# Performance work log

Measured on AMD Instinct MI355X. Metric: run time of the kernel, lower is better.

## Reference

```python
import jax, jax.numpy as jnp
import numpy as np

N_ENT, N_REL = 100000, 500
D1, D2 = 200, 200
OC, FW = 32, 9            # out_channels, filt_w (filt_h = 1, in_channels = 1)
B = 4096
W_IN = 2 * D1             # 400 = concat(e1, e2)
W_OUT = W_IN - FW + 1     # 392
FC_LEN = OC * W_OUT       # 12544
FC1_LEN = OC * FW         # 288
EPS = 1e-5


def setup_inputs() -> dict:
    key = jax.random.key(0)
    ks = jax.random.split(key, 8)
    return {
        "e1_idx": jax.random.randint(ks[0], (B,), 0, N_ENT),
        "r_idx": jax.random.randint(ks[1], (B,), 0, N_REL),
        "e2_idx": jax.random.randint(ks[2], (B,), 0, N_ENT),
        "E_table": jax.random.normal(ks[3], (N_ENT, D1), jnp.float32) * 0.1,
        "R_table": jax.random.normal(ks[4], (N_REL, D2), jnp.float32) * 0.1,
        "bn0_gamma": jnp.ones((1,), jnp.float32),
        "bn0_beta": jnp.zeros((1,), jnp.float32),
        "bn0_mean": jnp.zeros((1,), jnp.float32),
        "bn0_var": jnp.ones((1,), jnp.float32),
        "fc1_w": jax.random.normal(ks[5], (FC1_LEN, D2), jnp.float32) * 0.05,
        "fc1_b": jnp.zeros((FC1_LEN,), jnp.float32),
        "bn1_gamma": jnp.ones((OC,), jnp.float32),
        "bn1_beta": jnp.zeros((OC,), jnp.float32),
        "bn1_mean": jnp.zeros((OC,), jnp.float32),
        "bn1_var": jnp.ones((OC,), jnp.float32),
        "fc_w": jax.random.normal(ks[6], (W_IN, FC_LEN), jnp.float32) * 0.02,
        "fc_b": jnp.zeros((W_IN,), jnp.float32),
        "bn2_gamma": jnp.ones((W_IN,), jnp.float32),
        "bn2_beta": jnp.zeros((W_IN,), jnp.float32),
        "bn2_mean": jnp.zeros((W_IN,), jnp.float32),
        "bn2_var": jnp.ones((W_IN,), jnp.float32),
        "fc2_w": jax.random.normal(ks[7], (1, W_IN), jnp.float32) * 0.05,
        "fc2_b": jnp.zeros((1,), jnp.float32),
        "bias": jnp.zeros((1,), jnp.float32),
    }


def reference(e1_idx, r_idx, e2_idx, E_table, R_table,
              bn0_gamma, bn0_beta, bn0_mean, bn0_var,
              fc1_w, fc1_b,
              bn1_gamma, bn1_beta, bn1_mean, bn1_var,
              fc_w, fc_b,
              bn2_gamma, bn2_beta, bn2_mean, bn2_var,
              fc2_w, fc2_b, bias):
    # Embedding lookups; E = concat(e1, e2) along feature dim -> [B, 400]
    e1 = E_table[e1_idx]
    e2 = E_table[e2_idx]
    E = jnp.concatenate([e1, e2], axis=-1)

    # bn0 over the single input channel (eval-mode batchnorm)
    x = (E - bn0_mean[0]) * (bn0_gamma[0] / jnp.sqrt(bn0_var[0] + EPS)) + bn0_beta[0]

    # Hypernetwork: per-example conv filters [B, OC, FW]
    r = R_table[r_idx]
    k = (r @ fc1_w.T + fc1_b).reshape(-1, OC, FW)

    # Grouped (per-example) 1x9 convolution, valid padding.
    # Sliding windows: [B, W_OUT, FW] (loop over FW=9 taps only)
    xw = jnp.stack([x[:, j:j + W_OUT] for j in range(FW)], axis=-1)
    conv = jnp.einsum('bwj,boj->bow', xw, k)  # [B, OC, W_OUT]

    # bn1 over OC channels (eval mode)
    inv1 = bn1_gamma / jnp.sqrt(bn1_var + EPS)
    y = (conv - bn1_mean[None, :, None]) * inv1[None, :, None] + bn1_beta[None, :, None]

    # flatten in [B, OC, 1, W_OUT] contiguous order -> [B, OC*W_OUT]
    flat = y.reshape(y.shape[0], -1)

    h = flat @ fc_w.T + fc_b                                   # [B, 400]
    h = (h - bn2_mean) * (bn2_gamma / jnp.sqrt(bn2_var + EPS)) + bn2_beta
    out = jnp.tanh(h @ fc2_w.T + fc2_b) + bias                 # [B, 1]
    return out
```

## Files before the change

kernel.cpp:

```cpp
#include <hip/hip_runtime.h>

#define BATCH   4096
#define N_REL   500
#define D1      200
#define W_IN    400
#define OC      32
#define FW      9
#define W_OUT   392
#define FC_LEN  12544
#define FC1_LEN 288
#define EPS     1e-5f

#define OSPLIT  8
#define OCH     50
#define WBLK    49


__global__ __launch_bounds__(320)
void krel(const float* __restrict__ R, const float* __restrict__ fc1w,
          const float* __restrict__ fc1b,
          const float* __restrict__ g1, const float* __restrict__ v1,
          float* __restrict__ KR)
{
    __shared__ float rs[D1];
    const int rel = blockIdx.x;
    const int t = threadIdx.x;
    if (t < D1) rs[t] = R[(size_t)rel * D1 + t];
    __syncthreads();
    if (t < FC1_LEN) {
        const float4* wrow = (const float4*)(fc1w + (size_t)t * D1);
        float acc = fc1b[t];
        #pragma unroll 10
        for (int c = 0; c < D1 / 4; ++c) {
            float4 wv = wrow[c];
            acc += rs[c * 4 + 0] * wv.x + rs[c * 4 + 1] * wv.y
                 + rs[c * 4 + 2] * wv.z + rs[c * 4 + 3] * wv.w;
        }
        const int oc = t / FW;
        KR[(size_t)rel * FC1_LEN + t] = acc * (g1[oc] * rsqrtf(v1[oc] + EPS));
    }
}

__global__ __launch_bounds__(256)
void wpart_k(const float* __restrict__ fcw, const float* __restrict__ g2,
             const float* __restrict__ v2, const float* __restrict__ fc2w,
             float* __restrict__ wpart)
{
    __shared__ float wts[OCH];
    const int t = threadIdx.x;
    const int k = blockIdx.x * 256 + t;
    const int o0 = blockIdx.y * OCH;
    if (t < OCH) {
        const int o = o0 + t;
        wts[t] = fc2w[o] * g2[o] * rsqrtf(v2[o] + EPS);
    }
    __syncthreads();
    float acc = 0.f;
    #pragma unroll 10
    for (int i = 0; i < OCH; ++i)
        acc += fcw[(size_t)(o0 + i) * FC_LEN + k] * wts[i];
    wpart[blockIdx.y * FC_LEN + k] = acc;
}

__global__ __launch_bounds__(256)
void wsum_k(const float* __restrict__ wpart,
            const float* __restrict__ g1, const float* __restrict__ b1,
            const float* __restrict__ m1, const float* __restrict__ v1,
            const float* __restrict__ g2, const float* __restrict__ b2,
            const float* __restrict__ m2, const float* __restrict__ v2,
            const float* __restrict__ fcb, const float* __restrict__ fc2w,
            const float* __restrict__ fc2b,
            float* __restrict__ wbig, float* __restrict__ c3part)
{
    __shared__ float red[256];
    const int t = threadIdx.x;
    const int k = blockIdx.x * 256 + t;
    float w8 = 0.f;
    #pragma unroll
    for (int y = 0; y < OSPLIT; ++y) w8 += wpart[y * FC_LEN + k];
    wbig[k] = w8;
    const int oc = k / W_OUT;
    const float inv1 = g1[oc] * rsqrtf(v1[oc] + EPS);
    float pc = (b1[oc] - m1[oc] * inv1) * w8;
    if (blockIdx.x == 0) {
        for (int o = t; o < W_IN; o += 256) {
            const float s2 = g2[o] * rsqrtf(v2[o] + EPS);
            pc += (b2[o] - m2[o] * s2 + fcb[o] * s2) * fc2w[o];
        }
        if (t == 0) pc += fc2b[0];
    }
    red[t] = pc;
    __syncthreads();
    #pragma unroll
    for (int s = 128; s > 0; s >>= 1) {
        if (t < s) red[t] += red[t + s];
        __syncthreads();
    }
    if (t == 0) c3part[blockIdx.x] = red[0];
}

__global__ __launch_bounds__(256)
void prel_k(const float* __restrict__ KR, const float* __restrict__ wbig,
            const float* __restrict__ c3part,
            const float* __restrict__ g0, const float* __restrict__ b0,
            const float* __restrict__ m0p, const float* __restrict__ v0,
            float* __restrict__ Ps, float* __restrict__ crel)
{
    __shared__ __align__(16) float wls[FC_LEN];
    __shared__ float kfs[FC1_LEN];
    __shared__ float red[256];
    const int rel = blockIdx.x;
    const int t = threadIdx.x;

    for (int i = t; i < FC_LEN / 4; i += 256)
        *(float4*)(wls + i * 4) = *(const float4*)(wbig + i * 4);
    for (int i = t; i < FC1_LEN; i += 256)
        kfs[i] = KR[(size_t)rel * FC1_LEN + i];
    __syncthreads();

    const float s0 = g0[0] * rsqrtf(v0[0] + EPS);
    const float t0 = b0[0] - m0p[0] * s0;

    float lsum = 0.f;
    for (int d = t; d < W_IN; d += 256) {
        const int jlo = (d > W_OUT - 1) ? d - (W_OUT - 1) : 0;
        const int jhi = (d < FW - 1) ? d : (FW - 1);
        float p = 0.f;
        for (int oc = 0; oc < OC; ++oc) {
            const float* wb = wls + oc * W_OUT + d;
            const float* kk = kfs + oc * FW;
            for (int j = jlo; j <= jhi; ++j)
                p += kk[j] * wb[-j];
        }
        lsum += p;
        Ps[(size_t)rel * W_IN + d] = s0 * p;
    }
    red[t] = lsum;
    __syncthreads();
    #pragma unroll
    for (int s = 128; s > 0; s >>= 1) {
        if (t < s) red[t] += red[t + s];
        __syncthreads();
    }
    if (t == 0) {
        float cg = 0.f;
        for (int i = 0; i < WBLK; ++i) cg += c3part[i];
        crel[rel] = t0 * red[0] + cg;
    }
}

__global__ __launch_bounds__(256)
void final_k(const int* __restrict__ e1i, const int* __restrict__ ri,
             const int* __restrict__ e2i,
             const float* __restrict__ E, const float* __restrict__ Ps,
             const float* __restrict__ crel, const float* __restrict__ bias,
             float* __restrict__ out)
{
    const int wave = threadIdx.x >> 6, lane = threadIdx.x & 63;
    const int e = blockIdx.x * 4 + wave;
    const int i1 = e1i[e], i2 = e2i[e], rel = ri[e];
    const float* P  = Ps + (size_t)rel * W_IN;
    const float* E1 = E + (size_t)i1 * D1;
    const float* E2 = E + (size_t)i2 * D1;
    float acc = 0.f;
    for (int d = lane; d < D1; d += 64) acc += E1[d] * P[d];
    for (int d = lane; d < D1; d += 64) acc += E2[d] * P[D1 + d];
    #pragma unroll
    for (int off = 32; off > 0; off >>= 1) acc += __shfl_down(acc, off);
    if (lane == 0) out[e] = tanhf(acc + crel[rel]) + bias[0];
}

extern "C" void kernel_launch(void* const* d_in, const int* in_sizes, int n_in,
                              void* d_out, int out_size, void* d_ws, size_t ws_size,
                              hipStream_t stream)
{
    const int*   e1i  = (const int*)d_in[0];
    const int*   ri   = (const int*)d_in[1];
    const int*   e2i  = (const int*)d_in[2];
    const float* E    = (const float*)d_in[3];
    const float* R    = (const float*)d_in[4];
    const float* g0   = (const float*)d_in[5];
    const float* b0   = (const float*)d_in[6];
    const float* m0p  = (const float*)d_in[7];
    const float* v0   = (const float*)d_in[8];
    const float* fc1w = (const float*)d_in[9];
    const float* fc1b = (const float*)d_in[10];
    const float* g1   = (const float*)d_in[11];
    const float* b1   = (const float*)d_in[12];
    const float* m1   = (const float*)d_in[13];
    const float* v1   = (const float*)d_in[14];
    const float* fcw  = (const float*)d_in[15];
    const float* fcb  = (const float*)d_in[16];
    const float* g2   = (const float*)d_in[17];
    const float* b2   = (const float*)d_in[18];
    const float* m2   = (const float*)d_in[19];
    const float* v2   = (const float*)d_in[20];
    const float* fc2w = (const float*)d_in[21];
    const float* fc2b = (const float*)d_in[22];
    const float* bias = (const float*)d_in[23];

    char* ws = (char*)d_ws;
    float* KR     = (float*)(ws + 0);
    float* wpart  = (float*)(ws + 576000);
    float* wbig   = (float*)(ws + 977408);
    float* c3part = (float*)(ws + 1027584);
    float* Ps     = (float*)(ws + 1027840);
    float* crel   = (float*)(ws + 1827840);
    (void)ws_size; (void)in_sizes; (void)n_in; (void)out_size;

    krel<<<N_REL, 320, 0, stream>>>(R, fc1w, fc1b, g1, v1, KR);
    wpart_k<<<dim3(WBLK, OSPLIT), 256, 0, stream>>>(fcw, g2, v2, fc2w, wpart);
    wsum_k<<<WBLK, 256, 0, stream>>>(wpart, g1, b1, m1, v1, g2, b2, m2, v2,
                                     fcb, fc2w, fc2b, wbig, c3part);
    prel_k<<<N_REL, 256, 0, stream>>>(KR, wbig, c3part, g0, b0, m0p, v0, Ps, crel);
    final_k<<<BATCH / 4, 256, 0, stream>>>(e1i, ri, e2i, E, Ps, crel, bias,
                                           (float*)d_out);
}
```

Measured before the change: 211.2 us.

## Fuse five-stage pipeline into one cooperative persistent kernel with grid syncs

Replaces the five separate kernel launches with one cooperative kernel of 512 blocks that runs each stage in turn, separated by grid-wide syncs. The first stage interleaves the krel and wpart work units. The aim is to remove launch overhead and inter-kernel gaps. In exchange, every block carries about 52KB of shared memory, grid.sync has its own cost, and the later stages leave many blocks idle. The original multi-launch path is kept as a fallback if the cooperative launch fails.

```diff
diff --git a/kernel.cpp b/kernel.cpp
--- a/kernel.cpp
+++ b/kernel.cpp
@@ -1,4 +1,7 @@
 #include <hip/hip_runtime.h>
+#include <hip/hip_cooperative_groups.h>
+
+namespace cg = cooperative_groups;
 
 #define BATCH   4096
 #define N_REL   500
@@ -14,6 +17,152 @@
 #define OSPLIT  8
 #define OCH     50
 #define WBLK    49
+#define GRID    512
+
+
+struct Params {
+    const int *e1i, *ri, *e2i;
+    const float *E, *R;
+    const float *g0, *b0, *m0p, *v0;
+    const float *fc1w, *fc1b;
+    const float *g1, *b1, *m1, *v1;
+    const float *fcw, *fcb;
+    const float *g2, *b2, *m2, *v2;
+    const float *fc2w, *fc2b, *bias;
+    float *KR, *wpart, *wbig, *c3part, *Ps, *crel, *out;
+};
+
+__global__ __launch_bounds__(256)
+void fused_k(Params p)
+{
+    cg::grid_group grid = cg::this_grid();
+    __shared__ __align__(16) float smem[13088];
+    const int t  = threadIdx.x;
+    const int bx = blockIdx.x;
+
+    for (int u = bx; u < N_REL + OSPLIT * WBLK; u += GRID) {
+        if (u < N_REL) {
+            float* rs = smem;
+            if (t < D1) rs[t] = p.R[(size_t)u * D1 + t];
+            __syncthreads();
+            for (int i = t; i < FC1_LEN; i += 256) {
+                const float4* wrow = (const float4*)(p.fc1w + (size_t)i * D1);
+                float acc = p.fc1b[i];
+                #pragma unroll 10
+                for (int c = 0; c < D1 / 4; ++c) {
+                    float4 wv = wrow[c];
+                    acc += rs[c * 4 + 0] * wv.x + rs[c * 4 + 1] * wv.y
+                         + rs[c * 4 + 2] * wv.z + rs[c * 4 + 3] * wv.w;
+                }
+                const int oc = i / FW;
+                p.KR[(size_t)u * FC1_LEN + i] = acc * (p.g1[oc] * rsqrtf(p.v1[oc] + EPS));
+            }
+            __syncthreads();
+        } else {
+            const int v = u - N_REL;
+            const int y = v / WBLK, kb = v - y * WBLK;
+            const int o0 = y * OCH;
+            float* wts = smem;
+            if (t < OCH) {
+                const int o = o0 + t;
+                wts[t] = p.fc2w[o] * p.g2[o] * rsqrtf(p.v2[o] + EPS);
+            }
+            __syncthreads();
+            const int k = kb * 256 + t;
+            float acc = 0.f;
+            #pragma unroll 10
+            for (int i = 0; i < OCH; ++i)
+                acc += p.fcw[(size_t)(o0 + i) * FC_LEN + k] * wts[i];
+            p.wpart[y * FC_LEN + k] = acc;
+            __syncthreads();
+        }
+    }
+    grid.sync();
+
+    if (bx < WBLK) {
+        float* red = smem;
+        const int k = bx * 256 + t;
+        float w8 = 0.f;
+        #pragma unroll
+        for (int y = 0; y < OSPLIT; ++y) w8 += p.wpart[y * FC_LEN + k];
+        p.wbig[k] = w8;
+        const int oc = k / W_OUT;
+        const float inv1 = p.g1[oc] * rsqrtf(p.v1[oc] + EPS);
+        float pc = (p.b1[oc] - p.m1[oc] * inv1) * w8;
+        if (bx == 0) {
+            for (int o = t; o < W_IN; o += 256) {
+                const float s2 = p.g2[o] * rsqrtf(p.v2[o] + EPS);
+                pc += (p.b2[o] - p.m2[o] * s2 + p.fcb[o] * s2) * p.fc2w[o];
+            }
+            if (t == 0) pc += p.fc2b[0];
+        }
+        red[t] = pc;
+        __syncthreads();
+        #pragma unroll
+        for (int s = 128; s > 0; s >>= 1) {
+            if (t < s) red[t] += red[t + s];
+            __syncthreads();
+        }
+        if (t == 0) p.c3part[bx] = red[0];
+    }
+    grid.sync();
+
+    if (bx < N_REL) {
+        float* wls = smem;
+        float* kfs = smem + FC_LEN;
+        float* red = smem + FC_LEN + FC1_LEN;
+        for (int i = t; i < FC_LEN / 4; i += 256)
+            *(float4*)(wls + i * 4) = *(const float4*)(p.wbig + i * 4);
+        for (int i = t; i < FC1_LEN; i += 256)
+            kfs[i] = p.KR[(size_t)bx * FC1_LEN + i];
+        __syncthreads();
+
+        const float s0 = p.g0[0] * rsqrtf(p.v0[0] + EPS);
+        const float t0 = p.b0[0] - p.m0p[0] * s0;
+
+        float lsum = 0.f;
+        for (int d = t; d < W_IN; d += 256) {
+            const int jlo = (d > W_OUT - 1) ? d - (W_OUT - 1) : 0;
+            const int jhi = (d < FW - 1) ? d : (FW - 1);
+            float pp = 0.f;
+            for (int oc = 0; oc < OC; ++oc) {
+                const float* wb = wls + oc * W_OUT + d;
+                const float* kk = kfs + oc * FW;
+                for (int j = jlo; j <= jhi; ++j)
+                    pp += kk[j] * wb[-j];
+            }
+            lsum += pp;
+            p.Ps[(size_t)bx * W_IN + d] = s0 * pp;
+        }
+        red[t] = lsum;
+        __syncthreads();
+        #pragma unroll
+        for (int s = 128; s > 0; s >>= 1) {
+            if (t < s) red[t] += red[t + s];
+            __syncthreads();
+        }
+        if (t == 0) {
+            float cgs = 0.f;
+            for (int i = 0; i < WBLK; ++i) cgs += p.c3part[i];
+            p.crel[bx] = t0 * red[0] + cgs;
+        }
+    }
+    grid.sync();
+
+    const int wave = t >> 6, lane = t & 63;
+    for (int e = bx * 4 + wave; e < BATCH; e += GRID * 4) {
+        const int i1 = p.e1i[e], i2 = p.e2i[e], rel = p.ri[e];
+        const float* Pv = p.Ps + (size_t)rel * W_IN;
+        const float* E1 = p.E + (size_t)i1 * D1;
+        const float* E2 = p.E + (size_t)i2 * D1;
+        float acc = 0.f;
+        for (int d = lane; d < D1; d += 64)
+            acc += E1[d] * Pv[d] + E2[d] * Pv[D1 + d];
+        #pragma unroll
+        for (int off = 32; off > 0; off >>= 1) acc += __shfl_down(acc, off);
+        if (lane == 0) p.out[e] = tanhf(acc + p.crel[rel]) + p.bias[0];
+    }
+}
 
 
 __global__ __launch_bounds__(320)
@@ -125,15 +274,15 @@
     for (int d = t; d < W_IN; d += 256) {
         const int jlo = (d > W_OUT - 1) ? d - (W_OUT - 1) : 0;
         const int jhi = (d < FW - 1) ? d : (FW - 1);
-        float p = 0.f;
+        float pp = 0.f;
         for (int oc = 0; oc < OC; ++oc) {
             const float* wb = wls + oc * W_OUT + d;
             const float* kk = kfs + oc * FW;
             for (int j = jlo; j <= jhi; ++j)
-                p += kk[j] * wb[-j];
-        }
-        lsum += p;
-        Ps[(size_t)rel * W_IN + d] = s0 * p;
+                pp += kk[j] * wb[-j];
+        }
+        lsum += pp;
+        Ps[(size_t)rel * W_IN + d] = s0 * pp;
     }
     red[t] = lsum;
     __syncthreads();
@@ -143,9 +292,9 @@
         __syncthreads();
     }
     if (t == 0) {
-        float cg = 0.f;
-        for (int i = 0; i < WBLK; ++i) cg += c3part[i];
-        crel[rel] = t0 * red[0] + cg;
+        float cgs = 0.f;
+        for (int i = 0; i < WBLK; ++i) cgs += c3part[i];
+        crel[rel] = t0 * red[0] + cgs;
     }
 }
 
@@ -208,11 +357,23 @@
     float* crel   = (float*)(ws + 1827840);
     (void)ws_size; (void)in_sizes; (void)n_in; (void)out_size;
 
-    krel<<<N_REL, 320, 0, stream>>>(R, fc1w, fc1b, g1, v1, KR);
-    wpart_k<<<dim3(WBLK, OSPLIT), 256, 0, stream>>>(fcw, g2, v2, fc2w, wpart);
-    wsum_k<<<WBLK, 256, 0, stream>>>(wpart, g1, b1, m1, v1, g2, b2, m2, v2,
-                                     fcb, fc2w, fc2b, wbig, c3part);
-    prel_k<<<N_REL, 256, 0, stream>>>(KR, wbig, c3part, g0, b0, m0p, v0, Ps, crel);
-    final_k<<<BATCH / 4, 256, 0, stream>>>(e1i, ri, e2i, E, Ps, crel, bias,
-                                           (float*)d_out);
-}
+    Params prm = { e1i, ri, e2i, E, R, g0, b0, m0p, v0, fc1w, fc1b,
+                   g1, b1, m1, v1, fcw, fcb, g2, b2, m2, v2,
+                   fc2w, fc2b, bias,
+                   KR, wpart, wbig, c3part, Ps, crel, (float*)d_out };
+    void* args[] = { &prm };
+
+    hipError_t err = hipLaunchCooperativeKernel((const void*)fused_k,
+                                                dim3(GRID), dim3(256),
+                                                args, 0, stream);
+    if (err != hipSuccess) {
+        (void)hipGetLastError();
+        krel<<<N_REL, 320, 0, stream>>>(R, fc1w, fc1b, g1, v1, KR);
+        wpart_k<<<dim3(WBLK, OSPLIT), 256, 0, stream>>>(fcw, g2, v2, fc2w, wpart);
+        wsum_k<<<WBLK, 256, 0, stream>>>(wpart, g1, b1, m1, v1, g2, b2, m2, v2,
+                                         fcb, fc2w, fc2b, wbig, c3part);
+        prel_k<<<N_REL, 256, 0, stream>>>(KR, wbig, c3part, g0, b0, m0p, v0, Ps, crel);
+        final_k<<<BATCH / 4, 256, 0, stream>>>(e1i, ri, e2i, E, Ps, crel, bias,
+                                               (float*)d_out);
+    }
+}
```

Result: slower. 411.1 us (+94.6%).

## Merge independent precompute kernels and fuse per-relation projection with final scoring

Applied to the files above, without the earlier changes.

The relation-filter kernel and the fc-weight partial-reduction kernel become one launch that dispatches on block index. The per-relation projection kernel now also does the final scoring: each relation block scans all batch indices in chunks, builds a shared-memory list of examples whose relation matches, and computes their dot products against the projection row held in shared memory. This removes two launches and the global round trip for the per-relation rows. In exchange, every one of the 500 blocks reads the full 4096-entry relation index array, and the work per block is uneven.

```diff
diff --git a/kernel.cpp b/kernel.cpp
--- a/kernel.cpp
+++ b/kernel.cpp
@@ -14,52 +14,52 @@
 #define OSPLIT  8
 #define OCH     50
 #define WBLK    49
-
-
-__global__ __launch_bounds__(320)
-void krel(const float* __restrict__ R, const float* __restrict__ fc1w,
+#define CHUNK   512
+
+
+__global__ __launch_bounds__(256)
+void ab_k(const float* __restrict__ R, const float* __restrict__ fc1w,
           const float* __restrict__ fc1b,
           const float* __restrict__ g1, const float* __restrict__ v1,
-          float* __restrict__ KR)
-{
-    __shared__ float rs[D1];
-    const int rel = blockIdx.x;
-    const int t = threadIdx.x;
-    if (t < D1) rs[t] = R[(size_t)rel * D1 + t];
-    __syncthreads();
-    if (t < FC1_LEN) {
-        const float4* wrow = (const float4*)(fc1w + (size_t)t * D1);
-        float acc = fc1b[t];
+          const float* __restrict__ fcw, const float* __restrict__ g2,
+          const float* __restrict__ v2, const float* __restrict__ fc2w,
+          float* __restrict__ KR, float* __restrict__ wpart)
+{
+    __shared__ float sm[D1];
+    const int bx = blockIdx.x;
+    const int t  = threadIdx.x;
+
+    if (bx < N_REL) {
+        if (t < D1) sm[t] = R[(size_t)bx * D1 + t];
+        __syncthreads();
+        for (int i = t; i < FC1_LEN; i += 256) {
+            const float4* wrow = (const float4*)(fc1w + (size_t)i * D1);
+            float acc = fc1b[i];
+            #pragma unroll 10
+            for (int c = 0; c < D1 / 4; ++c) {
+                float4 wv = wrow[c];
+                acc += sm[c * 4 + 0] * wv.x + sm[c * 4 + 1] * wv.y
+                     + sm[c * 4 + 2] * wv.z + sm[c * 4 + 3] * wv.w;
+            }
+            const int oc = i / FW;
+            KR[(size_t)bx * FC1_LEN + i] = acc * (g1[oc] * rsqrtf(v1[oc] + EPS));
+        }
+    } else {
+        const int v = bx - N_REL;
+        const int y = v / WBLK, kb = v - y * WBLK;
+        const int o0 = y * OCH;
+        if (t < OCH) {
+            const int o = o0 + t;
+            sm[t] = fc2w[o] * g2[o] * rsqrtf(v2[o] + EPS);
+        }
+        __syncthreads();
+        const int k = kb * 256 + t;
+        float acc = 0.f;
         #pragma unroll 10
-        for (int c = 0; c < D1 / 4; ++c) {
-            float4 wv = wrow[c];
-            acc += rs[c * 4 + 0] * wv.x + rs[c * 4 + 1] * wv.y
-                 + rs[c * 4 + 2] * wv.z + rs[c * 4 + 3] * wv.w;
-        }
-        const int oc = t / FW;
-        KR[(size_t)rel * FC1_LEN + t] = acc * (g1[oc] * rsqrtf(v1[oc] + EPS));
-    }
-}
-
-__global__ __launch_bounds__(256)
-void wpart_k(const float* __restrict__ fcw, const float* __restrict__ g2,
-             const float* __restrict__ v2, const float* __restrict__ fc2w,
-             float* __restrict__ wpart)
-{
-    __shared__ float wts[OCH];
-    const int t = threadIdx.x;
-    const int k = blockIdx.x * 256 + t;
-    const int o0 = blockIdx.y * OCH;
-    if (t < OCH) {
-        const int o = o0 + t;
-        wts[t] = fc2w[o] * g2[o] * rsqrtf(v2[o] + EPS);
-    }
-    __syncthreads();
-    float acc = 0.f;
-    #pragma unroll 10
-    for (int i = 0; i < OCH; ++i)
-        acc += fcw[(size_t)(o0 + i) * FC_LEN + k] * wts[i];
-    wpart[blockIdx.y * FC_LEN + k] = acc;
+        for (int i = 0; i < OCH; ++i)
+            acc += fcw[(size_t)(o0 + i) * FC_LEN + k] * sm[i];
+        wpart[y * FC_LEN + k] = acc;
+    }
 }
 
 __global__ __launch_bounds__(256)
@@ -100,17 +100,26 @@
 }
 
 __global__ __launch_bounds__(256)
-void prel_k(const float* __restrict__ KR, const float* __restrict__ wbig,
-            const float* __restrict__ c3part,
-            const float* __restrict__ g0, const float* __restrict__ b0,
-            const float* __restrict__ m0p, const float* __restrict__ v0,
-            float* __restrict__ Ps, float* __restrict__ crel)
+void prelfin_k(const int* __restrict__ e1i, const int* __restrict__ ri,
+               const int* __restrict__ e2i, const float* __restrict__ E,
+               const float* __restrict__ KR, const float* __restrict__ wbig,
+               const float* __restrict__ c3part,
+               const float* __restrict__ g0, const float* __restrict__ b0,
+               const float* __restrict__ m0p, const float* __restrict__ v0,
+               const float* __restrict__ bias,
+               float* __restrict__ out)
 {
     __shared__ __align__(16) float wls[FC_LEN];
     __shared__ float kfs[FC1_LEN];
     __shared__ float red[256];
+    __shared__ float prow[W_IN];
+    __shared__ float crelS;
+    __shared__ int   list[CHUNK];
+    __shared__ int   cnt;
+
     const int rel = blockIdx.x;
     const int t = threadIdx.x;
+    const int wave = t >> 6, lane = t & 63;
 
     for (int i = t; i < FC_LEN / 4; i += 256)
         *(float4*)(wls + i * 4) = *(const float4*)(wbig + i * 4);
@@ -125,15 +134,15 @@
     for (int d = t; d < W_IN; d += 256) {
         const int jlo = (d > W_OUT - 1) ? d - (W_OUT - 1) : 0;
         const int jhi = (d < FW - 1) ? d : (FW - 1);
-        float p = 0.f;
+        float pp = 0.f;
         for (int oc = 0; oc < OC; ++oc) {
             const float* wb = wls + oc * W_OUT + d;
             const float* kk = kfs + oc * FW;
             for (int j = jlo; j <= jhi; ++j)
-                p += kk[j] * wb[-j];
-        }
-        lsum += p;
-        Ps[(size_t)rel * W_IN + d] = s0 * p;
+                pp += kk[j] * wb[-j];
+        }
+        lsum += pp;
+        prow[d] = s0 * pp;
     }
     red[t] = lsum;
     __syncthreads();
@@ -143,31 +152,38 @@
         __syncthreads();
     }
     if (t == 0) {
-        float cg = 0.f;
-        for (int i = 0; i < WBLK; ++i) cg += c3part[i];
-        crel[rel] = t0 * red[0] + cg;
-    }
-}
-
-__global__ __launch_bounds__(256)
-void final_k(const int* __restrict__ e1i, const int* __restrict__ ri,
-             const int* __restrict__ e2i,
-             const float* __restrict__ E, const float* __restrict__ Ps,
-             const float* __restrict__ crel, const float* __restrict__ bias,
-             float* __restrict__ out)
-{
-    const int wave = threadIdx.x >> 6, lane = threadIdx.x & 63;
-    const int e = blockIdx.x * 4 + wave;
-    const int i1 = e1i[e], i2 = e2i[e], rel = ri[e];
-    const float* P  = Ps + (size_t)rel * W_IN;
-    const float* E1 = E + (size_t)i1 * D1;
-    const float* E2 = E + (size_t)i2 * D1;
-    float acc = 0.f;
-    for (int d = lane; d < D1; d += 64) acc += E1[d] * P[d];
-    for (int d = lane; d < D1; d += 64) acc += E2[d] * P[D1 + d];
-    #pragma unroll
-    for (int off = 32; off > 0; off >>= 1) acc += __shfl_down(acc, off);
-    if (lane == 0) out[e] = tanhf(acc + crel[rel]) + bias[0];
+        float cgs = 0.f;
+        for (int i = 0; i < WBLK; ++i) cgs += c3part[i];
+        crelS = t0 * red[0] + cgs;
+    }
+    __syncthreads();
+
+    const float cr = crelS;
+    const float bi = bias[0];
+
+    for (int c0 = 0; c0 < BATCH; c0 += CHUNK) {
+        if (t == 0) cnt = 0;
+        __syncthreads();
+        for (int e = c0 + t; e < c0 + CHUNK; e += 256)
+            if (ri[e] == rel) {
+                const int idx = atomicAdd(&cnt, 1);
+                list[idx] = e;
+            }
+        __syncthreads();
+        const int n = cnt;
+        for (int q = wave; q < n; q += 4) {
+            const int e = list[q];
+            const float* E1 = E + (size_t)e1i[e] * D1;
+            const float* E2 = E + (size_t)e2i[e] * D1;
+            float acc = 0.f;
+            for (int d = lane; d < D1; d += 64) acc += E1[d] * prow[d];
+            for (int d = lane; d < D1; d += 64) acc += E2[d] * prow[D1 + d];
+            #pragma unroll
+            for (int off = 32; off > 0; off >>= 1) acc += __shfl_down(acc, off);
+            if (lane == 0) out[e] = tanhf(acc + cr) + bi;
+        }
+        __syncthreads();
+    }
 }
 
 extern "C" void kernel_launch(void* const* d_in, const int* in_sizes, int n_in,
@@ -204,15 +220,12 @@
     float* wpart  = (float*)(ws + 576000);
     float* wbig   = (float*)(ws + 977408);
     float* c3part = (float*)(ws + 1027584);
-    float* Ps     = (float*)(ws + 1027840);
-    float* crel   = (float*)(ws + 1827840);
     (void)ws_size; (void)in_sizes; (void)n_in; (void)out_size;
 
-    krel<<<N_REL, 320, 0, stream>>>(R, fc1w, fc1b, g1, v1, KR);
-    wpart_k<<<dim3(WBLK, OSPLIT), 256, 0, stream>>>(fcw, g2, v2, fc2w, wpart);
+    ab_k<<<N_REL + OSPLIT * WBLK, 256, 0, stream>>>(R, fc1w, fc1b, g1, v1,
+                                                    fcw, g2, v2, fc2w, KR, wpart);
     wsum_k<<<WBLK, 256, 0, stream>>>(wpart, g1, b1, m1, v1, g2, b2, m2, v2,
                                      fcb, fc2w, fc2b, wbig, c3part);
-    prel_k<<<N_REL, 256, 0, stream>>>(KR, wbig, c3part, g0, b0, m0p, v0, Ps, crel);
-    final_k<<<BATCH / 4, 256, 0, stream>>>(e1i, ri, e2i, E, Ps, crel, bias,
-                                           (float*)d_out);
-}
+    prelfin_k<<<N_REL, 256, 0, stream>>>(e1i, ri, e2i, E, KR, wbig, c3part,
+                                         g0, b0, m0p, v0, bias, (float*)d_out);
+}
```

Result: slower. 237.0 us (+12.2%).
